# Performance work log

Measured on AMD Instinct MI355X. Metric: run time of the kernel, lower is better.

The kernel has to match this reference:

```python
import jax, jax.numpy as jnp
import numpy as np
from jax import lax

N = 131072
E = 2097152
D = 128
B = 16
NC = 5
EPS = 1e-5


def setup_inputs() -> dict:
    key = jax.random.key(0)
    ks = jax.random.split(key, 32)
    inp = {
        'h': jax.random.normal(ks[0], (N, D), jnp.float32),
        'edge_w': jax.random.uniform(ks[1], (E,), jnp.float32),
        'src': jax.random.randint(ks[2], (E,), 0, N),
        'dst': jax.random.randint(ks[3], (E,), 0, N),
        'node_gid': jnp.sort(jax.random.randint(ks[4], (N,), 0, B)),
        'num_graphs': B,
    }
    s = 0.05
    inp['conv1_w'] = jax.random.normal(ks[5], (D, D, 3), jnp.float32) * s
    inp['conv1_b'] = jax.random.normal(ks[6], (D,), jnp.float32) * s
    inp['conv2_w'] = jax.random.normal(ks[7], (D, D, 3), jnp.float32) * s
    inp['conv2_b'] = jax.random.normal(ks[8], (D,), jnp.float32) * s
    inp['conv3_w'] = jax.random.normal(ks[9], (D, D, 3), jnp.float32) * s
    inp['conv3_b'] = jax.random.normal(ks[10], (D,), jnp.float32) * s
    inp['press_w'] = jax.random.normal(ks[11], (1, 3, 3), jnp.float32) * s
    inp['press_b'] = jax.random.normal(ks[12], (1,), jnp.float32) * s
    names = ['g11', 'g12', 'g13', 'g2', 'g3', 'g4']
    for i, nm in enumerate(names):
        inp[nm + '_w'] = jax.random.normal(ks[13 + 2 * i], (D, D), jnp.float32) * s
        inp[nm + '_b'] = jax.random.normal(ks[14 + 2 * i], (D,), jnp.float32) * s
    inp['bn_g'] = jnp.ones((D,), jnp.float32)
    inp['bn_b'] = jnp.zeros((D,), jnp.float32)
    inp['cls1_w'] = jax.random.normal(ks[25], (D, 3 * D), jnp.float32) * s
    inp['cls1_b'] = jax.random.normal(ks[26], (D,), jnp.float32) * s
    inp['cls2_w'] = jax.random.normal(ks[27], (NC, D), jnp.float32) * s
    inp['cls2_b'] = jax.random.normal(ks[28], (NC,), jnp.float32) * s
    return inp


def _conv1d_nodes(x, w, b, dil, pad):
    # x: [N, D] treated as a length-N 1D signal with D channels (as in original)
    y = lax.conv_general_dilated(x.T[None], w, window_strides=(1,),
                                 padding=[(pad, pad)], rhs_dilation=(dil,),
                                 dimension_numbers=('NCH', 'OIH', 'NCH'))
    return (y[0] + b[:, None]).T  # [N, D]


def _bn(x, g, b):
    mu = jnp.mean(x, axis=0)
    var = jnp.mean((x - mu) ** 2, axis=0)
    return (x - mu) * lax.rsqrt(var + EPS) * g + b


def _gconv(h, W, b, src, dst, ew, n):
    # DGL GraphConv norm='none': aggregate-first (in==out), msg = h[src]*ew, sum at dst, then @W + b
    msg = h[src] * ew[:, None]            # [E, D]
    agg = jax.ops.segment_sum(msg, dst, num_segments=n)
    return agg @ W + b


def reference(h, edge_w, src, dst, node_gid, num_graphs,
              conv1_w, conv1_b, conv2_w, conv2_b, conv3_w, conv3_b,
              press_w, press_b,
              g11_w, g11_b, g12_w, g12_b, g13_w, g13_b,
              g2_w, g2_b, g3_w, g3_b, g4_w, g4_b,
              bn_g, bn_b, cls1_w, cls1_b, cls2_w, cls2_b):
    n = h.shape[0]
    c1 = _conv1d_nodes(h, conv1_w, conv1_b, 1, 1)
    c2 = _conv1d_nodes(h, conv2_w, conv2_b, 2, 2)
    c3 = _conv1d_nodes(h, conv3_w, conv3_b, 3, 3)
    h01 = _bn(jax.nn.relu(c1) + c2, bn_g, bn_b)
    h02 = _bn(jax.nn.relu(c2) + c3, bn_g, bn_b)
    h03 = _bn(jax.nn.relu(c3) + c1, bn_g, bn_b)

    a1 = jax.nn.relu(_gconv(h01, g11_w, g11_b, src, dst, edge_w, n))
    a2 = jax.nn.relu(_gconv(h02, g12_w, g12_b, src, dst, edge_w, n))
    a3 = jax.nn.relu(_gconv(h03, g13_w, g13_b, src, dst, edge_w, n))
    stacked = jnp.stack([a1, a2, a3], axis=1)  # [N, 3, D]
    pressed = lax.conv_general_dilated(stacked, press_w, window_strides=(1,),
                                       padding=[(1, 1)],
                                       dimension_numbers=('NCH', 'OIH', 'NCH'))
    ac_h1 = pressed[:, 0, :] + press_b  # [N, D]
    ac_h1 = _bn(ac_h1, bn_g, bn_b)      # dropout is identity in eval

    ac_h2 = jax.nn.relu(_gconv(ac_h1, g2_w, g2_b, src, dst, edge_w, n))
    ac_h3 = jax.nn.relu(_gconv(ac_h2, g3_w, g3_b, src, dst, edge_w, n))
    ac_h4 = jax.nn.relu(_gconv(ac_h3, g4_w, g4_b, src, dst, edge_w, n))

    hg2 = jax.ops.segment_sum(ac_h2, node_gid, num_segments=num_graphs)
    hg3 = jax.ops.segment_sum(ac_h3, node_gid, num_segments=num_graphs)
    hg4 = jax.ops.segment_sum(ac_h4, node_gid, num_segments=num_graphs)
    hg = jnp.concatenate([hg2, hg3, hg4], axis=1)  # [B, 3D]
    out = (hg @ cls1_w.T + cls1_b) @ cls2_w.T + cls2_b  # [B, NC]
    return out
```

## Files before the change

kernel.cpp:

```cpp
#include <hip/hip_runtime.h>

#define NN 131072
#define NE 2097152

typedef unsigned short u16;
typedef unsigned int u32;
typedef __attribute__((ext_vector_type(8))) short bf16x8;
typedef __attribute__((ext_vector_type(4))) float f32x4;
typedef __attribute__((ext_vector_type(2))) float f32x2;

__device__ __forceinline__ float bf2f(u16 v) {
  unsigned u = ((unsigned)v) << 16;
  return __builtin_bit_cast(float, u);
}
__device__ __forceinline__ float blo(u32 v) {
  return __builtin_bit_cast(float, v << 16);
}
__device__ __forceinline__ float bhi(u32 v) {
  return __builtin_bit_cast(float, v & 0xffff0000u);
}
__device__ __forceinline__ u16 f2bf(float f) {
  unsigned u = __builtin_bit_cast(unsigned, f);
  unsigned r = (u + 0x7fffu + ((u >> 16) & 1u)) >> 16;
  return (u16)r;
}

#define WDQ 3.0518509475997192e-05f

#define H16_OFF 0ull
#define A_OFF 33554432ull
#define B_OFF 67108864ull
#define C_OFF 100663296ull
#define Z_OFF 134217728ull
#define CSR_OFF 167772160ull
#define RP_OFF 184549376ull
#define DEG_OFF 185077760ull
#define SW_OFF 185602048ull
#define BS_OFF 186126336ull
#define SUMS_OFF 186130432ull
#define HG_OFF 186134528ull
#define WT16_OFF 186159104ull
#define WP16_OFF 186472448ull
#define CP_OFF 186681344ull
#define SV_OFF 186683392ull
#define SHV_OFF 186685440ull

__global__ void zerok(int* __restrict__ deg, float* __restrict__ sw,
                      float* __restrict__ sums, float* __restrict__ hg) {
  int i = blockIdx.x * 256 + threadIdx.x;
  deg[i] = 0;
  sw[i] = 0.f;
  if (i < 1024) sums[i] = 0.f;
  if (i < 6144) hg[i] = 0.f;
}

__global__ void h2bf(const float* __restrict__ h, u16* __restrict__ o) {
  int i = blockIdx.x * 256 + threadIdx.x;
  float4 v0 = *(const float4*)(h + (size_t)i * 8);
  float4 v1 = *(const float4*)(h + (size_t)i * 8 + 4);
  ushort4 a, b;
  a.x = f2bf(v0.x); a.y = f2bf(v0.y); a.z = f2bf(v0.z); a.w = f2bf(v0.w);
  b.x = f2bf(v1.x); b.y = f2bf(v1.y); b.z = f2bf(v1.z); b.w = f2bf(v1.w);
  *(ushort4*)(o + (size_t)i * 8) = a;
  *(ushort4*)(o + (size_t)i * 8 + 4) = b;
}

__global__ void prep_wT16(const float* __restrict__ w1, const float* __restrict__ w2,
                          const float* __restrict__ w3, u16* __restrict__ wT) {
  int e = blockIdx.x * 256 + threadIdx.x;
  if (e >= 3 * 3 * 128 * 128) return;
  int o = e & 127;
  int i = (e >> 7) & 127;
  int ct = e >> 14;
  int t = ct % 3, c = ct / 3;
  const float* w = (c == 0) ? w1 : (c == 1) ? w2 : w3;
  wT[(size_t)(c * 3 + t) * 17408 + o * 136 + i] = f2bf(w[(o * 128 + i) * 3 + t]);
}

__global__ void wprep16(const float* __restrict__ W, const float* __restrict__ sv,
                        u16* __restrict__ Wt) {
  int e = blockIdx.x * 256 + threadIdx.x;
  int o = e & 127, i = e >> 7;
  float s = sv ? sv[i] : 1.f;
  Wt[o * 136 + i] = f2bf(s * W[i * 128 + o]);
}

__global__ void cprep(const float* __restrict__ W, const float* __restrict__ shv,
                      float* __restrict__ cp) {
  int j = threadIdx.x;
  float a = 0.f;
  for (int i = 0; i < 128; ++i) a += shv[i] * W[i * 128 + j];
  cp[j] = a;
}

__global__ void bnparam(const float* __restrict__ sums, const float* __restrict__ g,
                        const float* __restrict__ b, float* __restrict__ sv,
                        float* __restrict__ shv, int tensor0) {
  int t = tensor0 + blockIdx.x;
  int o = threadIdx.x;
  float mu = sums[t * 256 + o] / (float)NN;
  float var = sums[t * 256 + 128 + o] / (float)NN - mu * mu;
  float s = g[o] * rsqrtf(var + 1e-5f);
  sv[t * 128 + o] = s;
  shv[t * 128 + o] = b[o] - mu * s;
}

template <int TAPS, int DIL, int OUT8>
__global__ __launch_bounds__(256, 4) void mfma_gemm(const u16* __restrict__ x,
                                                    const u16* __restrict__ wt,
                                                    u16* __restrict__ z) {
  __shared__ u16 sh[17408];
  int tid = threadIdx.x;
  int lane = tid & 63, wave = tid >> 6;
  int n0 = blockIdx.x * 128;
  int m = lane & 15, quad = lane >> 4;
  int koff = quad * 8;
  f32x4 acc[2][8];
#pragma unroll
  for (int a = 0; a < 2; ++a)
#pragma unroll
    for (int b = 0; b < 8; ++b) acc[a][b] = (f32x4){0.f, 0.f, 0.f, 0.f};
  int rbase = n0 + wave * 32 + m;

  for (int t = 0; t < TAPS; ++t) {
    if (TAPS > 1) __syncthreads();
    for (int idx = tid; idx < 2176; idx += 256)
      ((uint4*)sh)[idx] = ((const uint4*)(wt + (size_t)t * 17408))[idx];
    __syncthreads();
    const int shift = (TAPS == 3) ? (t - 1) * DIL : 0;
#pragma unroll
    for (int ks = 0; ks < 4; ++ks) {
      bf16x8 af[2];
#pragma unroll
      for (int rt = 0; rt < 2; ++rt) {
        int row = rbase + rt * 16 + shift;
        if (TAPS == 3) {
          int rc = min(max(row, 0), NN - 1);
          bf16x8 v = *(const bf16x8*)(x + (size_t)rc * 128 + ks * 32 + koff);
          bf16x8 zz = {};
          af[rt] = (row >= 0 && row < NN) ? v : zz;
        } else {
          af[rt] = *(const bf16x8*)(x + (size_t)row * 128 + ks * 32 + koff);
        }
      }
#pragma unroll
      for (int ct = 0; ct < 8; ++ct) {
        bf16x8 bf = *(const bf16x8*)(sh + (ct * 16 + m) * 136 + ks * 32 + koff);
        acc[0][ct] =
            __builtin_amdgcn_mfma_f32_16x16x32_bf16(af[0], bf, acc[0][ct], 0, 0, 0);
        acc[1][ct] =
            __builtin_amdgcn_mfma_f32_16x16x32_bf16(af[1], bf, acc[1][ct], 0, 0, 0);
      }
    }
  }
  __syncthreads();
#pragma unroll
  for (int rt = 0; rt < 2; ++rt)
#pragma unroll
    for (int ct = 0; ct < 8; ++ct)
#pragma unroll
      for (int r = 0; r < 4; ++r) {
        int rowl = wave * 32 + rt * 16 + quad * 4 + r;
        sh[rowl * 136 + ct * 16 + m] = f2bf(acc[rt][ct][r]);
      }
  __syncthreads();
  if (OUT8) {
    unsigned char* z8 = (unsigned char*)z;
#pragma unroll
    for (int it = 0; it < 8; ++it) {
      int q = tid + it * 256;
      int row = q >> 4, g = q & 15;
      uint4 v = *(const uint4*)(sh + row * 136 + g * 8);
      int w0 = __builtin_amdgcn_cvt_pk_fp8_f32(blo(v.x), bhi(v.x), 0, false);
      w0 = __builtin_amdgcn_cvt_pk_fp8_f32(blo(v.y), bhi(v.y), w0, true);
      int w1 = __builtin_amdgcn_cvt_pk_fp8_f32(blo(v.z), bhi(v.z), 0, false);
      w1 = __builtin_amdgcn_cvt_pk_fp8_f32(blo(v.w), bhi(v.w), w1, true);
      uint2 st;
      st.x = (u32)w0;
      st.y = (u32)w1;
      *(uint2*)(z8 + (size_t)(n0 + row) * 128 + g * 8) = st;
    }
  } else {
#pragma unroll
    for (int it = 0; it < 8; ++it) {
      int q = tid + it * 256;
      int row = q >> 4, g = q & 15;
      uint4 v = *(const uint4*)(sh + row * 136 + g * 8);
      *(uint4*)(z + (size_t)(n0 + row) * 128 + g * 8) = v;
    }
  }
}

__global__ __launch_bounds__(256) void combine(u16* __restrict__ A, u16* __restrict__ B,
                                               u16* __restrict__ C,
                                               const float* __restrict__ b1,
                                               const float* __restrict__ b2,
                                               const float* __restrict__ b3,
                                               float* __restrict__ sums) {
  __shared__ float red[2 * 128 * 6];
  int tid = threadIdx.x;
  int o = tid & 127, half = tid >> 7;
  int n0 = blockIdx.x * 32 + half * 16;
  float bb1 = b1[o], bb2 = b2[o], bb3 = b3[o];
  float s1 = 0, q1 = 0, s2 = 0, q2 = 0, s3 = 0, q3 = 0;
  for (int j = 0; j < 16; ++j) {
    size_t idx = (size_t)(n0 + j) * 128 + o;
    float c1 = bf2f(A[idx]) + bb1, c2 = bf2f(B[idx]) + bb2, c3 = bf2f(C[idx]) + bb3;
    float v1 = fmaxf(c1, 0.f) + c2;
    float v2 = fmaxf(c2, 0.f) + c3;
    float v3 = fmaxf(c3, 0.f) + c1;
    A[idx] = f2bf(v1);
    B[idx] = f2bf(v2);
    C[idx] = f2bf(v3);
    s1 += v1; q1 += v1 * v1;
    s2 += v2; q2 += v2 * v2;
    s3 += v3; q3 += v3 * v3;
  }
  int ri = (half * 128 + o) * 6;
  red[ri + 0] = s1; red[ri + 1] = q1; red[ri + 2] = s2;
  red[ri + 3] = q2; red[ri + 4] = s3; red[ri + 5] = q3;
  __syncthreads();
  if (half == 0) {
    int rj = (128 + o) * 6;
    atomicAdd(&sums[0 * 256 + o], s1 + red[rj + 0]);
    atomicAdd(&sums[0 * 256 + 128 + o], q1 + red[rj + 1]);
    atomicAdd(&sums[1 * 256 + o], s2 + red[rj + 2]);
    atomicAdd(&sums[1 * 256 + 128 + o], q2 + red[rj + 3]);
    atomicAdd(&sums[2 * 256 + o], s3 + red[rj + 4]);
    atomicAdd(&sums[2 * 256 + 128 + o], q3 + red[rj + 5]);
  }
}

__global__ void deg_sw_k(const int* __restrict__ dst, const float* __restrict__ ew,
                         int* __restrict__ deg, float* __restrict__ sw) {
  int e = blockIdx.x * 256 + threadIdx.x;
  if (e < NE) {
    int d = dst[e];
    atomicAdd(&deg[d], 1);
    atomicAdd(&sw[d], ew[e]);
  }
}

__global__ void scan1(const int* __restrict__ deg, int* __restrict__ rp,
                      int* __restrict__ bs) {
  __shared__ int s[256];
  int t = threadIdx.x;
  int i = blockIdx.x * 256 + t;
  int v = deg[i];
  s[t] = v;
  for (int off = 1; off < 256; off <<= 1) {
    __syncthreads();
    int x = (t >= off) ? s[t - off] : 0;
    __syncthreads();
    s[t] += x;
  }
  rp[i] = s[t] - v;
  if (t == 255) bs[blockIdx.x] = s[255];
}

__global__ void scan2(int* __restrict__ bs) {
  __shared__ int s[512];
  int t = threadIdx.x;
  int v = bs[t];
  s[t] = v;
  for (int off = 1; off < 512; off <<= 1) {
    __syncthreads();
    int x = (t >= off) ? s[t - off] : 0;
    __syncthreads();
    s[t] += x;
  }
  bs[t] = s[t] - v;
}

__global__ void scan3(int* __restrict__ rp, const int* __restrict__ bs,
                      int* __restrict__ cur) {
  int i = blockIdx.x * 256 + threadIdx.x;
  int r = rp[i] + bs[blockIdx.x];
  rp[i] = r;
  cur[i] = r;
  if (i == 0) rp[NN] = NE;
}

__global__ void csr_fill(const int* __restrict__ src, const int* __restrict__ dst,
                         const float* __restrict__ ew, int* __restrict__ cur,
                         u32* __restrict__ csrP) {
  int e = blockIdx.x * 256 + threadIdx.x;
  if (e < NE) {
    int d = dst[e];
    int p = atomicAdd(&cur[d], 1);
    u32 q = (u32)(ew[e] * 32767.f + 0.5f);
    csrP[p] = (u32)src[e] | (q << 17);
  }
}

#define AB3 4
#define PKCAP 512
__global__ __launch_bounds__(256, 4) void agg3_press(
    const unsigned char* __restrict__ z1, const unsigned char* __restrict__ z2,
    const unsigned char* __restrict__ z3, const u32* __restrict__ csrP,
    const int* __restrict__ rp, const float* __restrict__ sw,
    const float* __restrict__ cp, const float* __restrict__ b1,
    const float* __restrict__ b2, const float* __restrict__ b3,
    const float* __restrict__ pw, const float* __restrict__ pb,
    u16* __restrict__ P, float* __restrict__ sums) {
  __shared__ u32 ls_pk[4][PKCAP];
  __shared__ u16 otile[4][16 * 128];
  __shared__ int ls_rp[4][17];
  __shared__ float ls_sw[4][16];
  int lane = threadIdx.x & 63, wave = threadIdx.x >> 6;
  int d0 = blockIdx.x * 64 + wave * 16;
  if (lane < 17) ls_rp[wave][lane] = rp[d0 + lane];
  if (lane < 16) ls_sw[wave][lane] = sw[d0 + lane];
  float c1x = cp[lane * 2], c1y = cp[lane * 2 + 1];
  float c2x = cp[128 + lane * 2], c2y = cp[128 + lane * 2 + 1];
  float c3x = cp[256 + lane * 2], c3y = cp[256 + lane * 2 + 1];
  float b1x = b1[lane * 2], b1y = b1[lane * 2 + 1];
  float b2x = b2[lane * 2], b2y = b2[lane * 2 + 1];
  float b3x = b3[lane * 2], b3y = b3[lane * 2 + 1];
  float w10 = pw[0], w11 = pw[1], w12 = pw[2];
  float w20 = pw[3], w21 = pw[4], w22 = pw[5];
  float w30 = pw[6], w31 = pw[7], w32 = pw[8];
  float pbv = pb[0];
  __syncthreads();
  int s0 = __builtin_amdgcn_readfirstlane(ls_rp[wave][0]);
  int e0 = __builtin_amdgcn_readfirstlane(ls_rp[wave][16]);
  u32 vob = (u32)(lane * 2);
  float ax1 = 0.f, ay1 = 0.f, ax2 = 0.f, ay2 = 0.f, ax3 = 0.f, ay3 = 0.f;
  float sx = 0.f, qx = 0.f, sy = 0.f, qy = 0.f;
  int ld = 0;
  int nb = __builtin_amdgcn_readfirstlane(ls_rp[wave][1]);

  auto flush = [&]() {
    float swd = ls_sw[wave][ld];
    float a1x = fmaxf(ax1 + c1x * swd + b1x, 0.f);
    float a1y = fmaxf(ay1 + c1y * swd + b1y, 0.f);
    float a2x = fmaxf(ax2 + c2x * swd + b2x, 0.f);
    float a2y = fmaxf(ay2 + c2y * swd + b2y, 0.f);
    float a3x = fmaxf(ax3 + c3x * swd + b3x, 0.f);
    float a3y = fmaxf(ay3 + c3y * swd + b3y, 0.f);
    float l1 = __shfl_up(a1y, 1); if (lane == 0) l1 = 0.f;
    float l2 = __shfl_up(a2y, 1); if (lane == 0) l2 = 0.f;
    float l3 = __shfl_up(a3y, 1); if (lane == 0) l3 = 0.f;
    float r1 = __shfl_down(a1x, 1); if (lane == 63) r1 = 0.f;
    float r2 = __shfl_down(a2x, 1); if (lane == 63) r2 = 0.f;
    float r3 = __shfl_down(a3x, 1); if (lane == 63) r3 = 0.f;
    float ox = w10 * l1 + w11 * a1x + w12 * a1y + w20 * l2 + w21 * a2x +
               w22 * a2y + w30 * l3 + w31 * a3x + w32 * a3y + pbv;
    float oy = w10 * a1x + w11 * a1y + w12 * r1 + w20 * a2x + w21 * a2y +
               w22 * r2 + w30 * a3x + w31 * a3y + w32 * r3 + pbv;
    u32 pk2 = ((u32)f2bf(oy) << 16) | (u32)f2bf(ox);
    *(u32*)&otile[wave][ld * 128 + lane * 2] = pk2;
    sx += ox; qx += ox * ox;
    sy += oy; qy += oy * oy;
    ax1 = ay1 = ax2 = ay2 = ax3 = ay3 = 0.f;
    ++ld;
    nb = __builtin_amdgcn_readfirstlane(ls_rp[wave][ld < 16 ? ld + 1 : 16]);
  };

#define PKRD3(PK, J0)                                 \
  _Pragma("unroll") for (int k = 0; k < AB3; ++k) {   \
    int jc = (J0) + k;                                \
    jc = jc < cnt ? jc : cntm1;                       \
    PK[k] = ls_pk[wave][jc];                          \
  }
#define ISSUE3(VA, VB, VC, WV, PK, J0)                \
  _Pragma("unroll") for (int k = 0; k < AB3; ++k) {   \
    u32 p = PK[k];                                    \
    u32 off = ((p & 0x1FFFFu) << 7) | vob;            \
    VA[k] = *(const u16*)(z1 + off);                  \
    VB[k] = *(const u16*)(z2 + off);                  \
    VC[k] = *(const u16*)(z3 + off);                  \
    WV[k] = ((J0) + k < cnt) ? (float)(p >> 17) * WDQ : 0.f; \
  }
#define CONS3(VA, VB, VC, WV, J0)                     \
  _Pragma("unroll") for (int k = 0; k < AB3; ++k) {   \
    if ((J0) + k < cnt) {                             \
      int jg = cs + (J0) + k;                         \
      while (jg >= nb) flush();                       \
    }                                                 \
    float w = WV[k];                                  \
    f32x2 d1 = __builtin_amdgcn_cvt_pk_f32_fp8((int)VA[k], false); \
    f32x2 d2 = __builtin_amdgcn_cvt_pk_f32_fp8((int)VB[k], false); \
    f32x2 d3 = __builtin_amdgcn_cvt_pk_f32_fp8((int)VC[k], false); \
    ax1 += d1.x * w; ay1 += d1.y * w;                 \
    ax2 += d2.x * w; ay2 += d2.y * w;                 \
    ax3 += d3.x * w; ay3 += d3.y * w;                 \
  }

  int cs = s0;
  while (cs < e0) {
    int ce = min(cs + PKCAP, e0);
    int cnt = ce - cs;
    int cntm1 = cnt - 1;
    for (int i = lane; i < cnt; i += 64) ls_pk[wave][i] = csrP[cs + i];
    u32 pkA[AB3], pkB[AB3];
    u32 vaA[AB3], vbA[AB3], vcA[AB3], vaB[AB3], vbB[AB3], vcB[AB3];
    float wvA[AB3], wvB[AB3];
    PKRD3(pkA, 0)
    ISSUE3(vaA, vbA, vcA, wvA, pkA, 0)
    PKRD3(pkA, AB3)
    int jb = 0;
    while (true) {
      PKRD3(pkB, jb + 2 * AB3)
      if (jb + AB3 < cnt) { ISSUE3(vaB, vbB, vcB, wvB, pkA, jb + AB3) }
      CONS3(vaA, vbA, vcA, wvA, jb)
      if (jb + AB3 >= cnt) break;
      PKRD3(pkA, jb + 3 * AB3)
      if (jb + 2 * AB3 < cnt) { ISSUE3(vaA, vbA, vcA, wvA, pkB, jb + 2 * AB3) }
      CONS3(vaB, vbB, vcB, wvB, jb + AB3)
      if (jb + 2 * AB3 >= cnt) break;
      jb += 2 * AB3;
    }
    cs = ce;
  }
#undef PKRD3
#undef ISSUE3
#undef CONS3
  while (ld < 16) flush();

  {
    const u16* srcl = &otile[wave][0];
    u16* dstg = P + (size_t)d0 * 128;
#pragma unroll
    for (int i = 0; i < 4; ++i) {
      uint4 v = *(const uint4*)(srcl + i * 512 + lane * 8);
      *(uint4*)(dstg + i * 512 + lane * 8) = v;
    }
  }
  __syncthreads();
  float* red = (float*)&otile[0][0];
  int base = wave * 256 + lane * 4;
  red[base] = sx; red[base + 1] = qx; red[base + 2] = sy; red[base + 3] = qy;
  __syncthreads();
  int t = threadIdx.x;
  if (t < 64) {
    float s0_ = 0, q0_ = 0, s1_ = 0, q1_ = 0;
#pragma unroll
    for (int w = 0; w < 4; ++w) {
      int rb = w * 256 + t * 4;
      s0_ += red[rb]; q0_ += red[rb + 1]; s1_ += red[rb + 2]; q1_ += red[rb + 3];
    }
    atomicAdd(&sums[768 + t * 2], s0_);
    atomicAdd(&sums[768 + 128 + t * 2], q0_);
    atomicAdd(&sums[768 + t * 2 + 1], s1_);
    atomicAdd(&sums[768 + 128 + t * 2 + 1], q1_);
  }
}

#define AB2 8
__global__ __launch_bounds__(256, 4) void agg2(const unsigned char* __restrict__ z,
                                               const u32* __restrict__ csrP,
                                               const int* __restrict__ rp,
                                               const float* __restrict__ sw,
                                               const float* __restrict__ cvec,
                                               const float* __restrict__ bvec,
                                               u16* __restrict__ out,
                                               const int* __restrict__ gid,
                                               float* __restrict__ hg, int coloff) {
  __shared__ u32 ls_pk[4][PKCAP];
  __shared__ u16 otile[4][16 * 128];
  __shared__ int ls_rp[4][17];
  __shared__ float ls_sw[4][16];
  __shared__ int ls_gid[4][16];
  int lane = threadIdx.x & 63, wave = threadIdx.x >> 6;
  int d0 = blockIdx.x * 64 + wave * 16;
  if (lane < 17) ls_rp[wave][lane] = rp[d0 + lane];
  if (lane < 16) {
    ls_sw[wave][lane] = sw[d0 + lane];
    ls_gid[wave][lane] = gid[d0 + lane];
  }
  float bx = bvec[lane * 2], by = bvec[lane * 2 + 1];
  float cx = cvec ? cvec[lane * 2] : 0.f;
  float cy = cvec ? cvec[lane * 2 + 1] : 0.f;
  __syncthreads();
  int s0 = __builtin_amdgcn_readfirstlane(ls_rp[wave][0]);
  int e0 = __builtin_amdgcn_readfirstlane(ls_rp[wave][16]);
  u32 vob = (u32)(lane * 2);
  float ax = 0.f, ay = 0.f;
  int ld = 0;
  int nb = __builtin_amdgcn_readfirstlane(ls_rp[wave][1]);

  auto flush = [&]() {
    float swd = ls_sw[wave][ld];
    float rx = fmaxf(ax + cx * swd + bx, 0.f);
    float ry = fmaxf(ay + cy * swd + by, 0.f);
    u32 pk2 = ((u32)f2bf(ry) << 16) | (u32)f2bf(rx);
    *(u32*)&otile[wave][ld * 128 + lane * 2] = pk2;
    ax = 0.f;
    ay = 0.f;
    ++ld;
    nb = __builtin_amdgcn_readfirstlane(ls_rp[wave][ld < 16 ? ld + 1 : 16]);
  };

#define PKRD1(PK, J0)                                 \
  _Pragma("unroll") for (int k = 0; k < AB2; ++k) {   \
    int jc = (J0) + k;                                \
    jc = jc < cnt ? jc : cntm1;                       \
    PK[k] = ls_pk[wave][jc];                          \
  }
#define ISSUE1(VA, WV, PK, J0)                        \
  _Pragma("unroll") for (int k = 0; k < AB2; ++k) {   \
    u32 p = PK[k];                                    \
    u32 off = ((p & 0x1FFFFu) << 7) | vob;            \
    VA[k] = *(const u16*)(z + off);                   \
    WV[k] = ((J0) + k < cnt) ? (float)(p >> 17) * WDQ : 0.f; \
  }
#define CONS1(VA, WV, J0)                             \
  _Pragma("unroll") for (int k = 0; k < AB2; ++k) {   \
    if ((J0) + k < cnt) {                             \
      int jg = cs + (J0) + k;                         \
      while (jg >= nb) flush();                       \
    }                                                 \
    float w = WV[k];                                  \
    f32x2 d = __builtin_amdgcn_cvt_pk_f32_fp8((int)VA[k], false); \
    ax += d.x * w;                                    \
    ay += d.y * w;                                    \
  }

  int cs = s0;
  while (cs < e0) {
    int ce = min(cs + PKCAP, e0);
    int cnt = ce - cs;
    int cntm1 = cnt - 1;
    for (int i = lane; i < cnt; i += 64) ls_pk[wave][i] = csrP[cs + i];
    u32 pkA[AB2], pkB[AB2];
    u32 vaA[AB2], vaB[AB2];
    float wvA[AB2], wvB[AB2];
    PKRD1(pkA, 0)
    ISSUE1(vaA, wvA, pkA, 0)
    PKRD1(pkA, AB2)
    int jb = 0;
    while (true) {
      PKRD1(pkB, jb + 2 * AB2)
      if (jb + AB2 < cnt) { ISSUE1(vaB, wvB, pkA, jb + AB2) }
      CONS1(vaA, wvA, jb)
      if (jb + AB2 >= cnt) break;
      PKRD1(pkA, jb + 3 * AB2)
      if (jb + 2 * AB2 < cnt) { ISSUE1(vaA, wvA, pkB, jb + 2 * AB2) }
      CONS1(vaB, wvB, jb + AB2)
      if (jb + 2 * AB2 >= cnt) break;
      jb += 2 * AB2;
    }
    cs = ce;
  }
#undef PKRD1
#undef ISSUE1
#undef CONS1
  while (ld < 16) flush();

  {
    const u16* srcl = &otile[wave][0];
    u16* dstg = out + (size_t)d0 * 128;
#pragma unroll
    for (int i = 0; i < 4; ++i) {
      uint4 v = *(const uint4*)(srcl + i * 512 + lane * 8);
      *(uint4*)(dstg + i * 512 + lane * 8) = v;
    }
  }
  {
    float runx = 0.f, runy = 0.f;
    int curg = __builtin_amdgcn_readfirstlane(ls_gid[wave][0]);
    for (int r = 0; r < 16; ++r) {
      u32 v = *(const u32*)&otile[wave][r * 128 + lane * 2];
      float rx = blo(v), ry = bhi(v);
      int gn = __builtin_amdgcn_readfirstlane(ls_gid[wave][r]);
      if (gn != curg) {
        atomicAdd(&hg[curg * 384 + coloff + lane * 2], runx);
        atomicAdd(&hg[curg * 384 + coloff + lane * 2 + 1], runy);
        runx = 0.f;
        runy = 0.f;
        curg = gn;
      }
      runx += rx;
      runy += ry;
    }
    atomicAdd(&hg[curg * 384 + coloff + lane * 2], runx);
    atomicAdd(&hg[curg * 384 + coloff + lane * 2 + 1], runy);
  }
}

__global__ void classifier(const float* __restrict__ hg, const float* __restrict__ w1,
                           const float* __restrict__ b1, const float* __restrict__ w2,
                           const float* __restrict__ b2, float* __restrict__ out) {
  __shared__ float sh_hg[16 * 384];
  __shared__ float sh_z[16 * 128];
  int t = threadIdx.x;
  for (int u = t; u < 16 * 384; u += 256) sh_hg[u] = hg[u];
  __syncthreads();
  for (int u = 0; u < 8; ++u) {
    int idx = t + u * 256;
    int b = idx >> 7, o = idx & 127;
    float a = b1[o];
    for (int i = 0; i < 384; ++i) a += sh_hg[b * 384 + i] * w1[o * 384 + i];
    sh_z[b * 128 + o] = a;
  }
  __syncthreads();
  if (t < 80) {
    int b = t / 5, c = t % 5;
    float a = b2[c];
    for (int i = 0; i < 128; ++i) a += sh_z[b * 128 + i] * w2[c * 128 + i];
    out[b * 5 + c] = a;
  }
}

extern "C" void kernel_launch(void* const* d_in, const int* in_sizes, int n_in,
                              void* d_out, int out_size, void* d_ws, size_t ws_size,
                              hipStream_t stream) {
  const float* h = (const float*)d_in[0];
  const float* edge_w = (const float*)d_in[1];
  const int* src = (const int*)d_in[2];
  const int* dst = (const int*)d_in[3];
  const int* gid = (const int*)d_in[4];
  const float* c1w = (const float*)d_in[6];
  const float* c1b = (const float*)d_in[7];
  const float* c2w = (const float*)d_in[8];
  const float* c2b = (const float*)d_in[9];
  const float* c3w = (const float*)d_in[10];
  const float* c3b = (const float*)d_in[11];
  const float* pw = (const float*)d_in[12];
  const float* pb = (const float*)d_in[13];
  const float* g11w = (const float*)d_in[14];
  const float* g11b = (const float*)d_in[15];
  const float* g12w = (const float*)d_in[16];
  const float* g12b = (const float*)d_in[17];
  const float* g13w = (const float*)d_in[18];
  const float* g13b = (const float*)d_in[19];
  const float* g2w = (const float*)d_in[20];
  const float* g2b = (const float*)d_in[21];
  const float* g3w = (const float*)d_in[22];
  const float* g3b = (const float*)d_in[23];
  const float* g4w = (const float*)d_in[24];
  const float* g4b = (const float*)d_in[25];
  const float* bng = (const float*)d_in[26];
  const float* bnb = (const float*)d_in[27];
  const float* cl1w = (const float*)d_in[28];
  const float* cl1b = (const float*)d_in[29];
  const float* cl2w = (const float*)d_in[30];
  const float* cl2b = (const float*)d_in[31];

  char* ws = (char*)d_ws;
  u16* H16 = (u16*)(ws + H16_OFF);
  u16* A = (u16*)(ws + A_OFF);
  u16* B = (u16*)(ws + B_OFF);
  u16* C = (u16*)(ws + C_OFF);
  unsigned char* F1 = (unsigned char*)(ws + H16_OFF);
  unsigned char* F2 = (unsigned char*)(ws + H16_OFF + 16777216);
  unsigned char* F3 = (unsigned char*)(ws + Z_OFF);
  u16* P = (u16*)(ws + A_OFF);
  u32* csrP = (u32*)(ws + CSR_OFF);
  int* rp = (int*)(ws + RP_OFF);
  int* deg = (int*)(ws + DEG_OFF);
  int* cur = deg;
  float* sw = (float*)(ws + SW_OFF);
  int* bs = (int*)(ws + BS_OFF);
  float* sums = (float*)(ws + SUMS_OFF);
  float* hg = (float*)(ws + HG_OFF);
  u16* wT16 = (u16*)(ws + WT16_OFF);
  u16* wP16 = (u16*)(ws + WP16_OFF);
  float* cp = (float*)(ws + CP_OFF);
  float* sv = (float*)(ws + SV_OFF);
  float* shv = (float*)(ws + SHV_OFF);
  float* outp = (float*)d_out;

  zerok<<<512, 256, 0, stream>>>(deg, sw, sums, hg);
  h2bf<<<8192, 256, 0, stream>>>(h, H16);
  prep_wT16<<<1728, 256, 0, stream>>>(c1w, c2w, c3w, wT16);
  wprep16<<<64, 256, 0, stream>>>(g3w, (const float*)nullptr, wP16 + 4 * 17408);
  wprep16<<<64, 256, 0, stream>>>(g4w, (const float*)nullptr, wP16 + 5 * 17408);

  mfma_gemm<3, 1, 0><<<1024, 256, 0, stream>>>(H16, wT16 + 0 * 52224, A);
  mfma_gemm<3, 2, 0><<<1024, 256, 0, stream>>>(H16, wT16 + 1 * 52224, B);
  mfma_gemm<3, 3, 0><<<1024, 256, 0, stream>>>(H16, wT16 + 2 * 52224, C);
  combine<<<4096, 256, 0, stream>>>(A, B, C, c1b, c2b, c3b, sums);

  deg_sw_k<<<8192, 256, 0, stream>>>(dst, edge_w, deg, sw);
  scan1<<<512, 256, 0, stream>>>(deg, rp, bs);
  scan2<<<1, 512, 0, stream>>>(bs);
  scan3<<<512, 256, 0, stream>>>(rp, bs, cur);
  csr_fill<<<8192, 256, 0, stream>>>(src, dst, edge_w, cur, csrP);

  bnparam<<<3, 128, 0, stream>>>(sums, bng, bnb, sv, shv, 0);
  wprep16<<<64, 256, 0, stream>>>(g11w, sv + 0 * 128, wP16 + 0 * 17408);
  cprep<<<1, 128, 0, stream>>>(g11w, shv + 0 * 128, cp + 0 * 128);
  wprep16<<<64, 256, 0, stream>>>(g12w, sv + 1 * 128, wP16 + 1 * 17408);
  cprep<<<1, 128, 0, stream>>>(g12w, shv + 1 * 128, cp + 1 * 128);
  wprep16<<<64, 256, 0, stream>>>(g13w, sv + 2 * 128, wP16 + 2 * 17408);
  cprep<<<1, 128, 0, stream>>>(g13w, shv + 2 * 128, cp + 2 * 128);

  mfma_gemm<1, 0, 1><<<1024, 256, 0, stream>>>(A, wP16 + 0 * 17408, (u16*)F1);
  mfma_gemm<1, 0, 1><<<1024, 256, 0, stream>>>(B, wP16 + 1 * 17408, (u16*)F2);
  mfma_gemm<1, 0, 1><<<1024, 256, 0, stream>>>(C, wP16 + 2 * 17408, (u16*)F3);
  agg3_press<<<2048, 256, 0, stream>>>(F1, F2, F3, csrP, rp, sw, cp, g11b, g12b,
                                       g13b, pw, pb, P, sums);

  bnparam<<<1, 128, 0, stream>>>(sums, bng, bnb, sv, shv, 3);
  wprep16<<<64, 256, 0, stream>>>(g2w, sv + 3 * 128, wP16 + 3 * 17408);
  cprep<<<1, 128, 0, stream>>>(g2w, shv + 3 * 128, cp + 3 * 128);

  mfma_gemm<1, 0, 1><<<1024, 256, 0, stream>>>(P, wP16 + 3 * 17408, (u16*)F1);
  agg2<<<2048, 256, 0, stream>>>(F1, csrP, rp, sw, cp + 3 * 128, g2b, B, gid, hg, 0);
  mfma_gemm<1, 0, 1><<<1024, 256, 0, stream>>>(B, wP16 + 4 * 17408, (u16*)F1);
  agg2<<<2048, 256, 0, stream>>>(F1, csrP, rp, sw, (const float*)nullptr, g3b, C, gid, hg, 128);
  mfma_gemm<1, 0, 1><<<1024, 256, 0, stream>>>(C, wP16 + 5 * 17408, (u16*)F1);
  agg2<<<2048, 256, 0, stream>>>(F1, csrP, rp, sw, (const float*)nullptr, g4b, A, gid, hg, 256);

  classifier<<<1, 256, 0, stream>>>(hg, cl1w, cl1b, cl2w, cl2b, outp);
}
```

Baseline: 1.392 ms.

## Record per-edge rank during degree count; derive weight sums in aggregation

The degree-counting kernel now stores each edge's atomic-returned rank within its destination. The CSR fill then computes slots as rp[d]+rank with no second atomic pass. The float atomic accumulation of per-node edge-weight sums is removed; each aggregation kernel instead sums the dequantized weights on the fly while it walks the edges. This cuts one full pass of atomics over 2M edges and the float atomics. The cost is a 4 MB rank buffer, and the weight sum now uses the quantized weights rather than the exact float ones.

After: 1.203 ms. 13.6% less time.

```diff
diff --git a/kernel.cpp b/kernel.cpp
--- a/kernel.cpp
+++ b/kernel.cpp
@@ -32,6 +32,7 @@
 #define B_OFF 67108864ull
 #define C_OFF 100663296ull
 #define Z_OFF 134217728ull
+#define RE_OFF 150994944ull
 #define CSR_OFF 167772160ull
 #define RP_OFF 184549376ull
 #define DEG_OFF 185077760ull
@@ -45,11 +46,10 @@
 #define SV_OFF 186683392ull
 #define SHV_OFF 186685440ull
 
-__global__ void zerok(int* __restrict__ deg, float* __restrict__ sw,
-                      float* __restrict__ sums, float* __restrict__ hg) {
+__global__ void zerok(int* __restrict__ deg, float* __restrict__ sums,
+                      float* __restrict__ hg) {
   int i = blockIdx.x * 256 + threadIdx.x;
   deg[i] = 0;
-  sw[i] = 0.f;
   if (i < 1024) sums[i] = 0.f;
   if (i < 6144) hg[i] = 0.f;
 }
@@ -231,13 +231,13 @@
   }
 }
 
-__global__ void deg_sw_k(const int* __restrict__ dst, const float* __restrict__ ew,
-                         int* __restrict__ deg, float* __restrict__ sw) {
+__global__ void deg_rank_k(const int* __restrict__ dst, int* __restrict__ deg,
+                           u16* __restrict__ re) {
   int e = blockIdx.x * 256 + threadIdx.x;
   if (e < NE) {
     int d = dst[e];
-    atomicAdd(&deg[d], 1);
-    atomicAdd(&sw[d], ew[e]);
+    int r = atomicAdd(&deg[d], 1);
+    re[e] = (u16)r;
   }
 }
 
@@ -272,22 +272,19 @@
   bs[t] = s[t] - v;
 }
 
-__global__ void scan3(int* __restrict__ rp, const int* __restrict__ bs,
-                      int* __restrict__ cur) {
+__global__ void scan3(int* __restrict__ rp, const int* __restrict__ bs) {
   int i = blockIdx.x * 256 + threadIdx.x;
-  int r = rp[i] + bs[blockIdx.x];
-  rp[i] = r;
-  cur[i] = r;
+  rp[i] = rp[i] + bs[blockIdx.x];
   if (i == 0) rp[NN] = NE;
 }
 
-__global__ void csr_fill(const int* __restrict__ src, const int* __restrict__ dst,
-                         const float* __restrict__ ew, int* __restrict__ cur,
-                         u32* __restrict__ csrP) {
+__global__ void csr_fill2(const int* __restrict__ src, const int* __restrict__ dst,
+                          const float* __restrict__ ew, const int* __restrict__ rp,
+                          const u16* __restrict__ re, u32* __restrict__ csrP) {
   int e = blockIdx.x * 256 + threadIdx.x;
   if (e < NE) {
     int d = dst[e];
-    int p = atomicAdd(&cur[d], 1);
+    int p = rp[d] + (int)re[e];
     u32 q = (u32)(ew[e] * 32767.f + 0.5f);
     csrP[p] = (u32)src[e] | (q << 17);
   }
@@ -298,7 +295,7 @@
 __global__ __launch_bounds__(256, 4) void agg3_press(
     const unsigned char* __restrict__ z1, const unsigned char* __restrict__ z2,
     const unsigned char* __restrict__ z3, const u32* __restrict__ csrP,
-    const int* __restrict__ rp, const float* __restrict__ sw,
+    const int* __restrict__ rp,
     const float* __restrict__ cp, const float* __restrict__ b1,
     const float* __restrict__ b2, const float* __restrict__ b3,
     const float* __restrict__ pw, const float* __restrict__ pb,
@@ -306,11 +303,9 @@
   __shared__ u32 ls_pk[4][PKCAP];
   __shared__ u16 otile[4][16 * 128];
   __shared__ int ls_rp[4][17];
-  __shared__ float ls_sw[4][16];
   int lane = threadIdx.x & 63, wave = threadIdx.x >> 6;
   int d0 = blockIdx.x * 64 + wave * 16;
   if (lane < 17) ls_rp[wave][lane] = rp[d0 + lane];
-  if (lane < 16) ls_sw[wave][lane] = sw[d0 + lane];
   float c1x = cp[lane * 2], c1y = cp[lane * 2 + 1];
   float c2x = cp[128 + lane * 2], c2y = cp[128 + lane * 2 + 1];
   float c3x = cp[256 + lane * 2], c3y = cp[256 + lane * 2 + 1];
@@ -326,12 +321,13 @@
   int e0 = __builtin_amdgcn_readfirstlane(ls_rp[wave][16]);
   u32 vob = (u32)(lane * 2);
   float ax1 = 0.f, ay1 = 0.f, ax2 = 0.f, ay2 = 0.f, ax3 = 0.f, ay3 = 0.f;
+  float wsum = 0.f;
   float sx = 0.f, qx = 0.f, sy = 0.f, qy = 0.f;
   int ld = 0;
   int nb = __builtin_amdgcn_readfirstlane(ls_rp[wave][1]);
 
   auto flush = [&]() {
-    float swd = ls_sw[wave][ld];
+    float swd = wsum;
     float a1x = fmaxf(ax1 + c1x * swd + b1x, 0.f);
     float a1y = fmaxf(ay1 + c1y * swd + b1y, 0.f);
     float a2x = fmaxf(ax2 + c2x * swd + b2x, 0.f);
@@ -353,6 +349,7 @@
     sx += ox; qx += ox * ox;
     sy += oy; qy += oy * oy;
     ax1 = ay1 = ax2 = ay2 = ax3 = ay3 = 0.f;
+    wsum = 0.f;
     ++ld;
     nb = __builtin_amdgcn_readfirstlane(ls_rp[wave][ld < 16 ? ld + 1 : 16]);
   };
@@ -379,6 +376,7 @@
       while (jg >= nb) flush();                       \
     }                                                 \
     float w = WV[k];                                  \
+    wsum += w;                                        \
     f32x2 d1 = __builtin_amdgcn_cvt_pk_f32_fp8((int)VA[k], false); \
     f32x2 d2 = __builtin_amdgcn_cvt_pk_f32_fp8((int)VB[k], false); \
     f32x2 d3 = __builtin_amdgcn_cvt_pk_f32_fp8((int)VC[k], false); \
@@ -451,7 +449,6 @@
 __global__ __launch_bounds__(256, 4) void agg2(const unsigned char* __restrict__ z,
                                                const u32* __restrict__ csrP,
                                                const int* __restrict__ rp,
-                                               const float* __restrict__ sw,
                                                const float* __restrict__ cvec,
                                                const float* __restrict__ bvec,
                                                u16* __restrict__ out,
@@ -460,15 +457,11 @@
   __shared__ u32 ls_pk[4][PKCAP];
   __shared__ u16 otile[4][16 * 128];
   __shared__ int ls_rp[4][17];
-  __shared__ float ls_sw[4][16];
   __shared__ int ls_gid[4][16];
   int lane = threadIdx.x & 63, wave = threadIdx.x >> 6;
   int d0 = blockIdx.x * 64 + wave * 16;
   if (lane < 17) ls_rp[wave][lane] = rp[d0 + lane];
-  if (lane < 16) {
-    ls_sw[wave][lane] = sw[d0 + lane];
-    ls_gid[wave][lane] = gid[d0 + lane];
-  }
+  if (lane < 16) ls_gid[wave][lane] = gid[d0 + lane];
   float bx = bvec[lane * 2], by = bvec[lane * 2 + 1];
   float cx = cvec ? cvec[lane * 2] : 0.f;
   float cy = cvec ? cvec[lane * 2 + 1] : 0.f;
@@ -476,18 +469,18 @@
   int s0 = __builtin_amdgcn_readfirstlane(ls_rp[wave][0]);
   int e0 = __builtin_amdgcn_readfirstlane(ls_rp[wave][16]);
   u32 vob = (u32)(lane * 2);
-  float ax = 0.f, ay = 0.f;
+  float ax = 0.f, ay = 0.f, wsum = 0.f;
   int ld = 0;
   int nb = __builtin_amdgcn_readfirstlane(ls_rp[wave][1]);
 
   auto flush = [&]() {
-    float swd = ls_sw[wave][ld];
-    float rx = fmaxf(ax + cx * swd + bx, 0.f);
-    float ry = fmaxf(ay + cy * swd + by, 0.f);
+    float rx = fmaxf(ax + cx * wsum + bx, 0.f);
+    float ry = fmaxf(ay + cy * wsum + by, 0.f);
     u32 pk2 = ((u32)f2bf(ry) << 16) | (u32)f2bf(rx);
     *(u32*)&otile[wave][ld * 128 + lane * 2] = pk2;
     ax = 0.f;
     ay = 0.f;
+    wsum = 0.f;
     ++ld;
     nb = __builtin_amdgcn_readfirstlane(ls_rp[wave][ld < 16 ? ld + 1 : 16]);
   };
@@ -512,6 +505,7 @@
       while (jg >= nb) flush();                       \
     }                                                 \
     float w = WV[k];                                  \
+    wsum += w;                                        \
     f32x2 d = __builtin_amdgcn_cvt_pk_f32_fp8((int)VA[k], false); \
     ax += d.x * w;                                    \
     ay += d.y * w;                                    \
@@ -646,12 +640,11 @@
   unsigned char* F1 = (unsigned char*)(ws + H16_OFF);
   unsigned char* F2 = (unsigned char*)(ws + H16_OFF + 16777216);
   unsigned char* F3 = (unsigned char*)(ws + Z_OFF);
+  u16* re = (u16*)(ws + RE_OFF);
   u16* P = (u16*)(ws + A_OFF);
   u32* csrP = (u32*)(ws + CSR_OFF);
   int* rp = (int*)(ws + RP_OFF);
   int* deg = (int*)(ws + DEG_OFF);
-  int* cur = deg;
-  float* sw = (float*)(ws + SW_OFF);
   int* bs = (int*)(ws + BS_OFF);
   float* sums = (float*)(ws + SUMS_OFF);
   float* hg = (float*)(ws + HG_OFF);
@@ -662,7 +655,7 @@
   float* shv = (float*)(ws + SHV_OFF);
   float* outp = (float*)d_out;
 
-  zerok<<<512, 256, 0, stream>>>(deg, sw, sums, hg);
+  zerok<<<512, 256, 0, stream>>>(deg, sums, hg);
   h2bf<<<8192, 256, 0, stream>>>(h, H16);
   prep_wT16<<<1728, 256, 0, stream>>>(c1w, c2w, c3w, wT16);
   wprep16<<<64, 256, 0, stream>>>(g3w, (const float*)nullptr, wP16 + 4 * 17408);
@@ -673,11 +666,11 @@
   mfma_gemm<3, 3, 0><<<1024, 256, 0, stream>>>(H16, wT16 + 2 * 52224, C);
   combine<<<4096, 256, 0, stream>>>(A, B, C, c1b, c2b, c3b, sums);
 
-  deg_sw_k<<<8192, 256, 0, stream>>>(dst, edge_w, deg, sw);
+  deg_rank_k<<<8192, 256, 0, stream>>>(dst, deg, re);
   scan1<<<512, 256, 0, stream>>>(deg, rp, bs);
   scan2<<<1, 512, 0, stream>>>(bs);
-  scan3<<<512, 256, 0, stream>>>(rp, bs, cur);
-  csr_fill<<<8192, 256, 0, stream>>>(src, dst, edge_w, cur, csrP);
+  scan3<<<512, 256, 0, stream>>>(rp, bs);
+  csr_fill2<<<8192, 256, 0, stream>>>(src, dst, edge_w, rp, re, csrP);
 
   bnparam<<<3, 128, 0, stream>>>(sums, bng, bnb, sv, shv, 0);
   wprep16<<<64, 256, 0, stream>>>(g11w, sv + 0 * 128, wP16 + 0 * 17408);
@@ -690,7 +683,7 @@
   mfma_gemm<1, 0, 1><<<1024, 256, 0, stream>>>(A, wP16 + 0 * 17408, (u16*)F1);
   mfma_gemm<1, 0, 1><<<1024, 256, 0, stream>>>(B, wP16 + 1 * 17408, (u16*)F2);
   mfma_gemm<1, 0, 1><<<1024, 256, 0, stream>>>(C, wP16 + 2 * 17408, (u16*)F3);
-  agg3_press<<<2048, 256, 0, stream>>>(F1, F2, F3, csrP, rp, sw, cp, g11b, g12b,
+  agg3_press<<<2048, 256, 0, stream>>>(F1, F2, F3, csrP, rp, cp, g11b, g12b,
                                        g13b, pw, pb, P, sums);
 
   bnparam<<<1, 128, 0, stream>>>(sums, bng, bnb, sv, shv, 3);
@@ -698,11 +691,11 @@
   cprep<<<1, 128, 0, stream>>>(g2w, shv + 3 * 128, cp + 3 * 128);
 
   mfma_gemm<1, 0, 1><<<1024, 256, 0, stream>>>(P, wP16 + 3 * 17408, (u16*)F1);
-  agg2<<<2048, 256, 0, stream>>>(F1, csrP, rp, sw, cp + 3 * 128, g2b, B, gid, hg, 0);
+  agg2<<<2048, 256, 0, stream>>>(F1, csrP, rp, cp + 3 * 128, g2b, B, gid, hg, 0);
   mfma_gemm<1, 0, 1><<<1024, 256, 0, stream>>>(B, wP16 + 4 * 17408, (u16*)F1);
-  agg2<<<2048, 256, 0, stream>>>(F1, csrP, rp, sw, (const float*)nullptr, g3b, C, gid, hg, 128);
+  agg2<<<2048, 256, 0, stream>>>(F1, csrP, rp, (const float*)nullptr, g3b, C, gid, hg, 128);
   mfma_gemm<1, 0, 1><<<1024, 256, 0, stream>>>(C, wP16 + 5 * 17408, (u16*)F1);
-  agg2<<<2048, 256, 0, stream>>>(F1, csrP, rp, sw, (const float*)nullptr, g4b, A, gid, hg, 256);
+  agg2<<<2048, 256, 0, stream>>>(F1, csrP, rp, (const float*)nullptr, g4b, A, gid, hg, 256);
 
   classifier<<<1, 256, 0, stream>>>(hg, cl1w, cl1b, cl2w, cl2b, outp);
 }
```
